# Optimization experiments

Measured on AMD Instinct MI355X. Metric: run time of the kernel, lower is better.

## Reference

```python
import jax, jax.numpy as jnp
import numpy as np

B, L, D_MODEL = 2, 2048, 1024
D_INNER, D_STATE, D_CONV, DT_RANK = 2048, 16, 4, 64


def setup_inputs() -> dict:
    key = jax.random.key(0)
    ks = jax.random.split(key, 20)
    g = lambda k, shape, s: (jax.random.normal(k, shape, jnp.float32) * s)
    A_init = jnp.log(jnp.broadcast_to(
        jnp.arange(1, D_STATE + 1, dtype=jnp.float32), (D_INNER, D_STATE)))
    inp = {
        "hidden": g(ks[0], (B, L, D_MODEL), 1.0),
        # tied across directions (bidirectional_weight_tie=True)
        "W_in": g(ks[1], (2 * D_INNER, D_MODEL), 0.02),
        "W_out": g(ks[2], (D_MODEL, D_INNER), 0.02),
        # forward-direction Mamba params
        "conv_w_f": g(ks[3], (D_INNER, D_CONV), 0.2),
        "conv_b_f": jnp.zeros((D_INNER,), jnp.float32),
        "W_x_f": g(ks[4], (DT_RANK + 2 * D_STATE, D_INNER), 0.02),
        "W_dt_f": g(ks[5], (D_INNER, DT_RANK), 0.05),
        "b_dt_f": jax.random.uniform(ks[6], (D_INNER,), jnp.float32, -5.0, -4.0),
        "A_log_f": A_init,
        "D_f": jnp.ones((D_INNER,), jnp.float32),
        # reverse-direction Mamba params
        "conv_w_r": g(ks[7], (D_INNER, D_CONV), 0.2),
        "conv_b_r": jnp.zeros((D_INNER,), jnp.float32),
        "W_x_r": g(ks[8], (DT_RANK + 2 * D_STATE, D_INNER), 0.02),
        "W_dt_r": g(ks[9], (D_INNER, DT_RANK), 0.05),
        "b_dt_r": jax.random.uniform(ks[10], (D_INNER,), jnp.float32, -5.0, -4.0),
        "A_log_r": A_init,
        "D_r": jnp.ones((D_INNER,), jnp.float32),
    }
    return inp


def _mamba_block(h, W_in, W_out, conv_w, conv_b, W_x, W_dt, b_dt, A_log, Dp):
    # h: (B, L, d_model)
    xz = jnp.einsum('bld,ed->ble', h, W_in)          # (B,L,2*d_inner)
    x, z = jnp.split(xz, 2, axis=-1)
    # depthwise causal conv over L
    ker = jnp.swapaxes(conv_w, 0, 1)[:, None, :]      # (d_conv,1,d_inner)
    xc = jax.lax.conv_general_dilated(
        x, ker, window_strides=(1,), padding=[(D_CONV - 1, 0)],
        dimension_numbers=('NWC', 'WIO', 'NWC'),
        feature_group_count=D_INNER) + conv_b
    u = jax.nn.silu(xc)                               # (B,L,d_inner)
    xdbl = jnp.einsum('bld,ed->ble', u, W_x)          # (B,L,r+2n)
    dt, Bm, Cm = jnp.split(xdbl, [DT_RANK, DT_RANK + D_STATE], axis=-1)
    delta = jax.nn.softplus(jnp.einsum('blr,dr->bld', dt, W_dt) + b_dt)
    A = -jnp.exp(A_log)                               # (d_inner,d_state)

    def step(hs, xs):
        d_t, B_t, C_t, u_t = xs                       # (B,di),(B,n),(B,n),(B,di)
        dA = jnp.exp(d_t[:, :, None] * A)             # (B,di,n)
        hs = hs * dA + (d_t * u_t)[:, :, None] * B_t[:, None, :]
        y_t = jnp.einsum('bdn,bn->bd', hs, C_t)
        return hs, y_t

    xs = (jnp.swapaxes(delta, 0, 1), jnp.swapaxes(Bm, 0, 1),
          jnp.swapaxes(Cm, 0, 1), jnp.swapaxes(u, 0, 1))
    h0 = jnp.zeros((h.shape[0], D_INNER, D_STATE), h.dtype)
    _, ys = jax.lax.scan(step, h0, xs)                # ys: (L,B,d_inner)
    y = jnp.swapaxes(ys, 0, 1) + u * Dp
    y = y * jax.nn.silu(z)
    return jnp.einsum('bld,od->blo', y, W_out)        # (B,L,d_model)


def reference(hidden, W_in, W_out,
              conv_w_f, conv_b_f, W_x_f, W_dt_f, b_dt_f, A_log_f, D_f,
              conv_w_r, conv_b_r, W_x_r, W_dt_r, b_dt_r, A_log_r, D_r):
    out_f = _mamba_block(hidden, W_in, W_out, conv_w_f, conv_b_f,
                         W_x_f, W_dt_f, b_dt_f, A_log_f, D_f)
    out_r = _mamba_block(jnp.flip(hidden, axis=1), W_in, W_out, conv_w_r,
                         conv_b_r, W_x_r, W_dt_r, b_dt_r, A_log_r, D_r)
    return out_f + jnp.flip(out_r, axis=1)            # bidirectional 'add'
```

## Files before the change

kernel.cpp:

```cpp
#include <hip/hip_runtime.h>
#include <hip/hip_bf16.h>
#include <math.h>

typedef unsigned short u16;
typedef __attribute__((ext_vector_type(8))) short short8_t;
typedef __attribute__((ext_vector_type(4))) float f32x4;

#define B_   2
#define L_   2048
#define DM_  1024
#define DI_  2048
#define DS_  16
#define DR_  64
#define G_   96
#define BL_  (B_*L_)
#define BLDI_ ((size_t)BL_*DI_)
#define BLG_  ((size_t)BL_*G_)
#define NSEG_ 64
#define SEG_  32
#define PSTR_ ((size_t)BL_*G_)

__device__ __forceinline__ float sigmoidf_(float x){ return 1.f/(1.f+__expf(-x)); }
__device__ __forceinline__ float siluf_(float x){ return x*sigmoidf_(x); }
__device__ __forceinline__ float softplusf_(float x){
    return fmaxf(x,0.f) + __logf(1.f + __expf(-fabsf(x)));
}
__device__ __forceinline__ float bf2f(u16 u){
    union{unsigned int i; float f;} c; c.i = ((unsigned int)u)<<16; return c.f;
}
__device__ __forceinline__ u16 f2bf(float v){
    __hip_bfloat16 h = __float2bfloat16(v); return *(u16*)&h;
}
__device__ __forceinline__ void gll16(const void* g, void* l){
    __builtin_amdgcn_global_load_lds(
        (const __attribute__((address_space(1))) unsigned int*)g,
        (__attribute__((address_space(3))) unsigned int*)l, 16, 0, 0);
}
#define SCHUNK(lane) ((((lane) & 3) - (((lane) >> 3) & 3)) & 3)

__global__ __launch_bounds__(256) void f2ball_kernel(
    const float* __restrict__ p0, u16* __restrict__ q0,
    const float* __restrict__ p1, u16* __restrict__ q1,
    const float* __restrict__ p2, u16* __restrict__ q2,
    const float* __restrict__ p3, u16* __restrict__ q3,
    const float* __restrict__ p4, u16* __restrict__ q4,
    const float* __restrict__ p5, u16* __restrict__ q5,
    const float* __restrict__ p6, u16* __restrict__ q6)
{
    unsigned i = blockIdx.x*256 + threadIdx.x;
    const float* src; u16* dst; unsigned j;
    if      (i < 1048576u)            { src=p0; dst=q0; j=i; }
    else if (i < 2097152u)            { src=p1; dst=q1; j=i-1048576u; }
    else if (i < 2146304u)            { src=p2; dst=q2; j=i-2097152u; }
    else if (i < 2195456u)            { src=p3; dst=q3; j=i-2146304u; }
    else if (i < 2228224u)            { src=p4; dst=q4; j=i-2195456u; }
    else if (i < 2260992u)            { src=p5; dst=q5; j=i-2228224u; }
    else                              { src=p6; dst=q6; j=i-2260992u; }
    float4 v = *(const float4*)(src + (size_t)j*4);
    u16 t[4] = { f2bf(v.x), f2bf(v.y), f2bf(v.z), f2bf(v.w) };
    *(ushort4*)(dst + (size_t)j*4) = *(const ushort4*)t;
}

#define ABUF_ (128*64)
#define TBUF_ (ABUF_ + 256*64)

template<int C0, int C1>
__device__ __forceinline__ void stage256(
    const u16* __restrict__ A, int lda,
    const u16* __restrict__ B, int ldb,
    int m0, int n0, int k0, u16* buf,
    int wave, int lr, int cg)
{
    #pragma unroll
    for (int c = C0; c < C1; ++c) {
        if (c < 2) {
            const int r = wave*16 + c*8;
            gll16(A + (size_t)(m0 + r + lr)*lda + k0 + cg, buf + r*64);
        } else {
            const int r = wave*32 + (c-2)*8;
            gll16(B + (size_t)(n0 + r + lr)*ldb + k0 + cg, buf + ABUF_ + r*64);
        }
    }
}

__global__ __launch_bounds__(512, 2) void gemm256(
    const u16* __restrict__ A, int lda,
    const u16* __restrict__ B, int ldb,
    u16* __restrict__ C2, float* __restrict__ Cf, size_t cfZStr,
    int ldc, int K)
{
    __shared__ __align__(16) u16 lds3[3][TBUF_];

    const int tid  = threadIdx.x;
    const int wave = tid >> 6, lane = tid & 63;
    const int quad = lane >> 4, l16 = lane & 15;
    const int wm = wave >> 2, wn = wave & 3;
    const int m0 = blockIdx.y * 128, n0 = blockIdx.x * 256;
    const int nk = K >> 6;
    const int ks = blockIdx.z;
    A += (size_t)ks * K;
    B += (size_t)ks * K;

    const int lr  = lane >> 3;
    const int cg  = ((lane & 7) ^ lr) << 3;
    const int csw = l16 & 7;

    f32x4 acc[4][4];
    #pragma unroll
    for (int i = 0; i < 4; ++i)
        #pragma unroll
        for (int j = 0; j < 4; ++j) acc[i][j] = (f32x4){0.f,0.f,0.f,0.f};

    stage256<0,6>(A, lda, B, ldb, m0, n0, 0, lds3[0], wave, lr, cg);
    if (nk > 1)
        stage256<0,6>(A, lda, B, ldb, m0, n0, 64, lds3[1], wave, lr, cg);

    for (int t = 0; t < nk; ++t) {
        const u16* rb = lds3[t % 3];
        u16* sb = lds3[(t + 2) % 3];
        const int k2 = (t + 2) << 6;

        __builtin_amdgcn_sched_barrier(0);
        if (t + 1 < nk) asm volatile("s_waitcnt vmcnt(6)" ::: "memory");
        else            asm volatile("s_waitcnt vmcnt(0)" ::: "memory");
        __builtin_amdgcn_sched_barrier(0);
        __builtin_amdgcn_s_barrier();

        short8_t af[4][2], bf[4][2];
        #pragma unroll
        for (int i = 0; i < 4; ++i)
            #pragma unroll
            for (int kk = 0; kk < 2; ++kk)
                af[i][kk] = *(const short8_t*)
                    &rb[(wm*64 + i*16 + l16)*64 + (((kk*4+quad)^csw)<<3)];
        #pragma unroll
        for (int j = 0; j < 2; ++j)
            #pragma unroll
            for (int kk = 0; kk < 2; ++kk)
                bf[j][kk] = *(const short8_t*)
                    &rb[ABUF_ + (wn*64 + j*16 + l16)*64 + (((kk*4+quad)^csw)<<3)];
        if (t + 2 < nk)
            stage256<0,3>(A, lda, B, ldb, m0, n0, k2, sb, wave, lr, cg);
        asm volatile("s_waitcnt lgkmcnt(0)" ::: "memory");
        __builtin_amdgcn_sched_barrier(0);
        __builtin_amdgcn_s_setprio(1);
        #pragma unroll
        for (int i = 0; i < 4; ++i)
            #pragma unroll
            for (int j = 0; j < 2; ++j)
                #pragma unroll
                for (int kk = 0; kk < 2; ++kk)
                    acc[i][j] = __builtin_amdgcn_mfma_f32_16x16x32_bf16(
                                    bf[j][kk], af[i][kk], acc[i][j], 0, 0, 0);
        __builtin_amdgcn_s_setprio(0);
        __builtin_amdgcn_s_barrier();

        #pragma unroll
        for (int j = 2; j < 4; ++j)
            #pragma unroll
            for (int kk = 0; kk < 2; ++kk)
                bf[j][kk] = *(const short8_t*)
                    &rb[ABUF_ + (wn*64 + j*16 + l16)*64 + (((kk*4+quad)^csw)<<3)];
        if (t + 2 < nk)
            stage256<3,6>(A, lda, B, ldb, m0, n0, k2, sb, wave, lr, cg);
        asm volatile("s_waitcnt lgkmcnt(0)" ::: "memory");
        __builtin_amdgcn_sched_barrier(0);
        __builtin_amdgcn_s_setprio(1);
        #pragma unroll
        for (int i = 0; i < 4; ++i)
            #pragma unroll
            for (int j = 2; j < 4; ++j)
                #pragma unroll
                for (int kk = 0; kk < 2; ++kk)
                    acc[i][j] = __builtin_amdgcn_mfma_f32_16x16x32_bf16(
                                    bf[j][kk], af[i][kk], acc[i][j], 0, 0, 0);
        __builtin_amdgcn_s_setprio(0);
    }

    if (Cf) {
        float* dst = Cf + (size_t)ks*cfZStr;
        #pragma unroll
        for (int i = 0; i < 4; ++i) {
            const int row = m0 + wm*64 + i*16 + l16;
            #pragma unroll
            for (int j = 0; j < 4; ++j) {
                const int col = n0 + wn*64 + j*16 + quad*4;
                *(float4*)&dst[(size_t)row*ldc + col] =
                    make_float4(acc[i][j][0], acc[i][j][1],
                                acc[i][j][2], acc[i][j][3]);
            }
        }
    } else {
        #pragma unroll
        for (int i = 0; i < 4; ++i) {
            const int row = m0 + wm*64 + i*16 + l16;
            #pragma unroll
            for (int j = 0; j < 4; ++j) {
                const int col = n0 + wn*64 + j*16 + quad*4;
                u16 t4[4] = { f2bf(acc[i][j][0]), f2bf(acc[i][j][1]),
                              f2bf(acc[i][j][2]), f2bf(acc[i][j][3]) };
                *(ushort4*)&C2[(size_t)row*ldc + col] = *(const ushort4*)t4;
            }
        }
    }
}

__global__ __launch_bounds__(256) void wred_kernel(
    const float* __restrict__ P, float* __restrict__ out)
{
    unsigned i = blockIdx.x*256 + threadIdx.x;
    size_t o = (size_t)i*4;
    float4 a = *(const float4*)&P[o];
    float4 b = *(const float4*)&P[o + (size_t)BL_*DM_];
    a.x += b.x; a.y += b.y; a.z += b.z; a.w += b.w;
    *(float4*)&out[o] = a;
}

__global__ __launch_bounds__(256) void gemm_mfma(
    const u16* __restrict__ A, int lda, size_t aStr,
    const u16* __restrict__ B, int ldb, size_t bStr,
    float* __restrict__ C, int ldc, size_t cStr,
    u16* __restrict__ C2,
    int M, int N, int K,
    const float* __restrict__ bias0, const float* __restrict__ bias1, int epi)
{
    __shared__ u16 Al[128*32];
    __shared__ u16 Bl[128*32];

    const int dir = blockIdx.z;
    A += (size_t)dir*aStr; B += (size_t)dir*bStr;
    if (C)  C  += (size_t)dir*cStr;
    if (C2) C2 += (size_t)dir*cStr;
    const float* bias = dir ? bias1 : bias0;

    const int tid  = threadIdx.x;
    const int wave = tid >> 6, lane = tid & 63;
    const int wm = (wave >> 1) * 64, wn = (wave & 1) * 64;
    const int m0 = blockIdx.y * 128, n0 = blockIdx.x * 128;
    const int quad = lane >> 4, l16 = lane & 15;

    const int srow = lane >> 2;
    const int scol = SCHUNK(lane) * 8;
    const int rc0  = ((quad + (l16 >> 1)) & 3) * 8;

    f32x4 acc[4][4];
    #pragma unroll
    for (int i = 0; i < 4; ++i)
        #pragma unroll
        for (int j = 0; j < 4; ++j) acc[i][j] = (f32x4){0.f,0.f,0.f,0.f};

    for (int k0 = 0; k0 < K; k0 += 32) {
        __syncthreads();
        #pragma unroll
        for (int j = 0; j < 2; ++j) {
            const int g   = wave*2 + j;
            const int row = g*16 + srow;
            gll16(A + (size_t)(m0 + row)*lda + k0 + scol, &Al[g*16*32]);
            gll16(B + (size_t)(n0 + row)*ldb + k0 + scol, &Bl[g*16*32]);
        }
        __syncthreads();

        short8_t af[4], bf[4];
        #pragma unroll
        for (int i = 0; i < 4; ++i) {
            af[i] = *(const short8_t*)&Al[(wm + i*16 + l16)*32 + rc0];
            bf[i] = *(const short8_t*)&Bl[(wn + i*16 + l16)*32 + rc0];
        }
        #pragma unroll
        for (int i = 0; i < 4; ++i)
            #pragma unroll
            for (int j = 0; j < 4; ++j)
                acc[i][j] = __builtin_amdgcn_mfma_f32_16x16x32_bf16(
                                bf[j], af[i], acc[i][j], 0, 0, 0);
    }

    #pragma unroll
    for (int i = 0; i < 4; ++i) {
        const int row = m0 + wm + i*16 + l16;
        #pragma unroll
        for (int j = 0; j < 4; ++j) {
            const int col = n0 + wn + j*16 + quad*4;
            if (col < N) {
                float4 o = make_float4(acc[i][j][0], acc[i][j][1],
                                       acc[i][j][2], acc[i][j][3]);
                if (epi) {
                    float4 bb = *(const float4*)&bias[col];
                    o.x = softplusf_(o.x + bb.x);
                    o.y = softplusf_(o.y + bb.y);
                    o.z = softplusf_(o.z + bb.z);
                    o.w = softplusf_(o.w + bb.w);
                }
                if (C) *(float4*)&C[(size_t)row*ldc + col] = o;
                if (C2) {
                    u16 t[4] = { f2bf(o.x), f2bf(o.y), f2bf(o.z), f2bf(o.w) };
                    *(ushort4*)&C2[(size_t)row*ldc + col] = *(const ushort4*)t;
                }
            }
        }
    }
}

__global__ __launch_bounds__(256) void gemm_mfma64(
    const u16* __restrict__ A, int lda, size_t aStr,
    const u16* __restrict__ B, int ldb, size_t bStr,
    float* __restrict__ C, int ldc, size_t cZStr,
    int M, int N, int Ksub, int KS)
{
    __shared__ u16 Al[64*32];
    __shared__ u16 Bl[128*32];

    const int z = blockIdx.z;
    const int dir = z / KS, ks = z - dir*KS;
    A += (size_t)dir*aStr + (size_t)ks*Ksub;
    B += (size_t)dir*bStr + (size_t)ks*Ksub;
    C += (size_t)z*cZStr;

    const int tid  = threadIdx.x;
    const int wave = tid >> 6, lane = tid & 63;
    const int m0 = blockIdx.y * 64, n0 = blockIdx.x * 128;
    const int quad = lane >> 4, l16 = lane & 15;
    const int wn = wave * 32;

    const int srow = lane >> 2;
    const int scol = SCHUNK(lane) * 8;
    const int rc0  = ((quad + (l16 >> 1)) & 3) * 8;

    f32x4 acc[4][2];
    #pragma unroll
    for (int i = 0; i < 4; ++i)
        #pragma unroll
        for (int j = 0; j < 2; ++j) acc[i][j] = (f32x4){0.f,0.f,0.f,0.f};

    for (int k0 = 0; k0 < Ksub; k0 += 32) {
        __syncthreads();
        gll16(A + (size_t)(m0 + wave*16 + srow)*lda + k0 + scol, &Al[wave*16*32]);
        #pragma unroll
        for (int j = 0; j < 2; ++j) {
            const int g = wave*2 + j;
            gll16(B + (size_t)(n0 + g*16 + srow)*ldb + k0 + scol, &Bl[g*16*32]);
        }
        __syncthreads();

        short8_t af[4], bf[2];
        #pragma unroll
        for (int i = 0; i < 4; ++i)
            af[i] = *(const short8_t*)&Al[(i*16 + l16)*32 + rc0];
        #pragma unroll
        for (int j = 0; j < 2; ++j)
            bf[j] = *(const short8_t*)&Bl[(wn + j*16 + l16)*32 + rc0];
        #pragma unroll
        for (int i = 0; i < 4; ++i)
            #pragma unroll
            for (int j = 0; j < 2; ++j)
                acc[i][j] = __builtin_amdgcn_mfma_f32_16x16x32_bf16(
                                bf[j], af[i], acc[i][j], 0, 0, 0);
    }

    #pragma unroll
    for (int i = 0; i < 4; ++i) {
        const int row = m0 + i*16 + l16;
        #pragma unroll
        for (int j = 0; j < 2; ++j) {
            const int col = n0 + wn + j*16 + quad*4;
            if (col < N) {
                float4 o = make_float4(acc[i][j][0], acc[i][j][1],
                                       acc[i][j][2], acc[i][j][3]);
                *(float4*)&C[(size_t)row*ldc + col] = o;
            }
        }
    }
}

__global__ __launch_bounds__(256) void xred_kernel(
    const float* __restrict__ P, float* __restrict__ XD, u16* __restrict__ XDb)
{
    unsigned i = blockIdx.x*256 + threadIdx.x;
    unsigned c4  = i % 24;
    unsigned row = (i / 24) & 4095;
    unsigned dir = i / (24*4096);
    size_t o = (size_t)row*G_ + c4*4;
    size_t pb = (size_t)dir*4*PSTR_ + o;

    float4 s = *(const float4*)&P[pb];
    #pragma unroll
    for (int ks = 1; ks < 4; ++ks) {
        float4 v = *(const float4*)&P[pb + (size_t)ks*PSTR_];
        s.x += v.x; s.y += v.y; s.z += v.z; s.w += v.w;
    }
    *(float4*)&XD[(size_t)dir*BLG_ + o] = s;
    u16 t[4] = { f2bf(s.x), f2bf(s.y), f2bf(s.z), f2bf(s.w) };
    *(ushort4*)&XDb[(size_t)dir*BLG_ + o] = *(const ushort4*)t;
}

#define LPT_ 8
__global__ __launch_bounds__(256) void conv_silu_kernel(
    const u16* __restrict__ xz,
    const float* __restrict__ wf, const float* __restrict__ bf_,
    const float* __restrict__ wr, const float* __restrict__ br_,
    u16* __restrict__ ub)
{
    unsigned i = blockIdx.x*256 + threadIdx.x;
    int d0  = (i & 511) << 2;
    int lg  = (i >> 9) & 255;
    int b   = (i >> 17) & 1;
    int dir = (int)(i >> 18);

    const float* wv = dir ? wr : wf;
    const float* bv = dir ? br_ : bf_;
    float4 bias = *(const float4*)(bv + d0);
    float4 w0 = *(const float4*)(wv + (d0+0)*4);
    float4 w1 = *(const float4*)(wv + (d0+1)*4);
    float4 w2 = *(const float4*)(wv + (d0+2)*4);
    float4 w3 = *(const float4*)(wv + (d0+3)*4);

    const int l0 = lg * LPT_;
    const size_t xb = (size_t)b*L_*4096 + d0;

    float h0[4], h1[4], h2[4];
    #pragma unroll
    for (int c = 0; c < 4; ++c) { h0[c]=0.f; h1[c]=0.f; h2[c]=0.f; }
    if (lg > 0) {
        #pragma unroll
        for (int k = 0; k < 3; ++k) {
            int j = l0 - 3 + k;
            int row = dir ? (L_-1-j) : j;
            uint2 xr = *(const uint2*)(&xz[xb + (size_t)row*4096]);
            const u16* xp = (const u16*)&xr;
            float* h = (k==0) ? h0 : ((k==1) ? h1 : h2);
            h[0]=bf2f(xp[0]); h[1]=bf2f(xp[1]); h[2]=bf2f(xp[2]); h[3]=bf2f(xp[3]);
        }
    }

    size_t off = (((size_t)dir*B_ + b)*L_ + l0)*DI_ + d0;
    #pragma unroll
    for (int t = 0; t < LPT_; ++t) {
        int j = l0 + t;
        int row = dir ? (L_-1-j) : j;
        uint2 xr = *(const uint2*)(&xz[xb + (size_t)row*4096]);
        const u16* xp = (const u16*)&xr;
        float c0 = bf2f(xp[0]), c1 = bf2f(xp[1]);
        float c2 = bf2f(xp[2]), c3 = bf2f(xp[3]);
        float a0 = bias.x + h0[0]*w0.x + h1[0]*w0.y + h2[0]*w0.z + c0*w0.w;
        float a1 = bias.y + h0[1]*w1.x + h1[1]*w1.y + h2[1]*w1.z + c1*w1.w;
        float a2 = bias.z + h0[2]*w2.x + h1[2]*w2.y + h2[2]*w2.z + c2*w2.w;
        float a3 = bias.w + h0[3]*w3.x + h1[3]*w3.y + h2[3]*w3.z + c3*w3.w;
        u16 t4[4] = { f2bf(siluf_(a0)), f2bf(siluf_(a1)),
                      f2bf(siluf_(a2)), f2bf(siluf_(a3)) };
        *(ushort4*)(ub + off) = *(const ushort4*)t4;
        off += DI_;
        #pragma unroll
        for (int c = 0; c < 4; ++c) { h0[c]=h1[c]; h1[c]=h2[c]; }
        h2[0]=c0; h2[1]=c1; h2[2]=c2; h2[3]=c3;
    }
}

__device__ __forceinline__ void scan_ld16(
    const u16* __restrict__ dp, const u16* __restrict__ up, int c,
    u16 (&dr)[16], u16 (&ur)[16])
{
    #pragma unroll
    for (int j = 0; j < 16; ++j) {
        dr[j] = dp[(size_t)((c<<4)+j)*DI_];
        ur[j] = up[(size_t)((c<<4)+j)*DI_];
    }
}

__device__ __forceinline__ void scanA_chunk16(
    const u16 (&dr)[16], const u16 (&ur)[16], int rbase,
    float (&h)[16], float& sumd, const float (*sB)[DS_])
{
    #pragma unroll
    for (int li = 0; li < 16; ++li) {
        const int row = rbase + li;
        float dlt = bf2f(dr[li]);
        float du  = dlt * bf2f(ur[li]);
        sumd += dlt;
        float e1 = __expf(-dlt);
        float e2 = e1*e1, e3 = e2*e1, e4 = e2*e2;
        float g5 = e1*e4, g6 = e2*e4, g7 = e3*e4, g8 = e4*e4;
        float g9 = e1*g8, g10 = e2*g8, g11 = e3*g8, g12 = e4*g8;
        float g13 = g5*g8, g14 = g6*g8, g15 = g7*g8, g16 = g8*g8;
        const float4* bp = (const float4*)&sB[row][0];
        float4 B0 = bp[0], B1 = bp[1], B2 = bp[2], B3 = bp[3];
        h[0]  = h[0] *e1  + du*B0.x;  h[1]  = h[1] *e2  + du*B0.y;
        h[2]  = h[2] *e3  + du*B0.z;  h[3]  = h[3] *e4  + du*B0.w;
        h[4]  = h[4] *g5  + du*B1.x;  h[5]  = h[5] *g6  + du*B1.y;
        h[6]  = h[6] *g7  + du*B1.z;  h[7]  = h[7] *g8  + du*B1.w;
        h[8]  = h[8] *g9  + du*B2.x;  h[9]  = h[9] *g10 + du*B2.y;
        h[10] = h[10]*g11 + du*B2.z;  h[11] = h[11]*g12 + du*B2.w;
        h[12] = h[12]*g13 + du*B3.x;  h[13] = h[13]*g14 + du*B3.y;
        h[14] = h[14]*g15 + du*B3.z;  h[15] = h[15]*g16 + du*B3.w;
    }
}

__device__ __forceinline__ void scanB_chunk16(
    const u16 (&dr)[16], const u16 (&ur)[16], int rbase,
    float (&h)[16], const float (*sB)[DS_], const float (*sC)[DS_],
    u16* __restrict__ yp)
{
    #pragma unroll
    for (int li = 0; li < 16; ++li) {
        const int row = rbase + li;
        float dlt = bf2f(dr[li]);
        float du  = dlt * bf2f(ur[li]);
        float e1 = __expf(-dlt);
        float e2 = e1*e1, e3 = e2*e1, e4 = e2*e2;
        float g5 = e1*e4, g6 = e2*e4, g7 = e3*e4, g8 = e4*e4;
        float g9 = e1*g8, g10 = e2*g8, g11 = e3*g8, g12 = e4*g8;
        float g13 = g5*g8, g14 = g6*g8, g15 = g7*g8, g16 = g8*g8;
        const float4* bp = (const float4*)&sB[row][0];
        const float4* cp = (const float4*)&sC[row][0];
        float4 B0 = bp[0], B1 = bp[1], B2 = bp[2], B3 = bp[3];
        float4 C0 = cp[0], C1 = cp[1], C2v = cp[2], C3 = cp[3];
        h[0]  = h[0] *e1  + du*B0.x;  h[1]  = h[1] *e2  + du*B0.y;
        h[2]  = h[2] *e3  + du*B0.z;  h[3]  = h[3] *e4  + du*B0.w;
        h[4]  = h[4] *g5  + du*B1.x;  h[5]  = h[5] *g6  + du*B1.y;
        h[6]  = h[6] *g7  + du*B1.z;  h[7]  = h[7] *g8  + du*B1.w;
        h[8]  = h[8] *g9  + du*B2.x;  h[9]  = h[9] *g10 + du*B2.y;
        h[10] = h[10]*g11 + du*B2.z;  h[11] = h[11]*g12 + du*B2.w;
        h[12] = h[12]*g13 + du*B3.x;  h[13] = h[13]*g14 + du*B3.y;
        h[14] = h[14]*g15 + du*B3.z;  h[15] = h[15]*g16 + du*B3.w;
        float y0 = h[0]*C0.x  + h[1]*C0.y  + h[2]*C0.z  + h[3]*C0.w;
        float y1 = h[4]*C1.x  + h[5]*C1.y  + h[6]*C1.z  + h[7]*C1.w;
        float y2 = h[8]*C2v.x + h[9]*C2v.y + h[10]*C2v.z+ h[11]*C2v.w;
        float y3 = h[12]*C3.x + h[13]*C3.y + h[14]*C3.z + h[15]*C3.w;
        yp[(size_t)row*DI_] = f2bf((y0+y1)+(y2+y3));
    }
}

__global__ __launch_bounds__(256) void scan_passA(
    const u16* __restrict__ ub,
    const u16* __restrict__ db,
    const float* __restrict__ xdbl,
    float* __restrict__ Hend, float* __restrict__ Sd)
{
    __shared__ float sB[SEG_][DS_];

    const int bx  = blockIdx.x;
    const int seg = bx & 63, dg = (bx >> 6) & 7, pair = bx >> 9;
    const int tid = threadIdx.x;
    const int d   = (dg << 8) + tid;
    const int lseg = seg * SEG_;
    const size_t base  = (size_t)pair * L_ * DI_;
    const size_t xbase = (size_t)pair * L_ * G_;

    const u16* dp = db + base + (size_t)lseg*DI_ + d;
    const u16* up = ub + base + (size_t)lseg*DI_ + d;

    u16 dr0[16], ur0[16], dr1[16], ur1[16];
    scan_ld16(dp, up, 0, dr0, ur0);
    scan_ld16(dp, up, 1, dr1, ur1);

    #pragma unroll
    for (int k = 0; k < 2; ++k) {
        int idx = (k << 8) + tid;
        sB[idx >> 4][idx & 15] =
            xdbl[xbase + (size_t)(lseg + (idx >> 4))*G_ + 64 + (idx & 15)];
    }

    float h[16];
    #pragma unroll
    for (int n = 0; n < 16; ++n) h[n] = 0.f;
    float sumd = 0.f;
    __syncthreads();

    scanA_chunk16(dr0, ur0,  0, h, sumd, sB);
    scanA_chunk16(dr1, ur1, 16, h, sumd, sB);

    const size_t ho = ((size_t)(seg*4 + pair)*2048 + d)*16;
    #pragma unroll
    for (int r = 0; r < 4; ++r)
        *(float4*)&Hend[ho + r*4] = make_float4(h[r*4],h[r*4+1],h[r*4+2],h[r*4+3]);
    Sd[(size_t)(seg*4 + pair)*2048 + d] = sumd;
}

__global__ __launch_bounds__(256) void scan_fixup(
    const float* __restrict__ Hend, const float* __restrict__ Sd,
    float* __restrict__ Hin,
    const float* __restrict__ A_log_f, const float* __restrict__ A_log_r)
{
    int idx = blockIdx.x*256 + threadIdx.x;
    int n = idx & 15, d = (idx >> 4) & 2047, pair = idx >> 15;
    int dir = pair >> 1;
    float a = -__expf((dir ? A_log_r : A_log_f)[d*16 + n]);
    float hin = 0.f;
    #pragma unroll
    for (int s = 0; s < NSEG_; ++s) {
        size_t o = ((size_t)(s*4 + pair)*2048 + d)*16 + n;
        Hin[o] = hin;
        float P = __expf(a * Sd[(size_t)(s*4 + pair)*2048 + d]);
        hin = Hend[o] + P*hin;
    }
}

__global__ __launch_bounds__(256) void scan_passB(
    const u16* __restrict__ ub,
    const u16* __restrict__ db,
    const float* __restrict__ xdbl,
    const float* __restrict__ Hin,
    u16* __restrict__ yb)
{
    __shared__ float sB[SEG_][DS_];
    __shared__ float sC[SEG_][DS_];

    const int bx  = blockIdx.x;
    const int seg = bx & 63, dg = (bx >> 6) & 7, pair = bx >> 9;
    const int tid = threadIdx.x;
    const int d   = (dg << 8) + tid;
    const int lseg = seg * SEG_;
    const size_t base  = (size_t)pair * L_ * DI_;
    const size_t xbase = (size_t)pair * L_ * G_;

    const u16* dp = db + base + (size_t)lseg*DI_ + d;
    const u16* up = ub + base + (size_t)lseg*DI_ + d;
    u16*       yp = yb + base + (size_t)lseg*DI_ + d;

    u16 dr0[16], ur0[16], dr1[16], ur1[16];
    scan_ld16(dp, up, 0, dr0, ur0);
    scan_ld16(dp, up, 1, dr1, ur1);

    #pragma unroll
    for (int k = 0; k < 2; ++k) {
        int idx = (k << 8) + tid;
        int row = idx >> 4, col = idx & 15;
        const float* src = &xdbl[xbase + (size_t)(lseg + row)*G_ + 64 + col];
        sB[row][col] = src[0];
        sC[row][col] = src[16];
    }

    float h[16];
    const size_t ho = ((size_t)(seg*4 + pair)*2048 + d)*16;
    #pragma unroll
    for (int r = 0; r < 4; ++r) {
        float4 v = *(const float4*)&Hin[ho + r*4];
        h[r*4]=v.x; h[r*4+1]=v.y; h[r*4+2]=v.z; h[r*4+3]=v.w;
    }
    __syncthreads();

    scanB_chunk16(dr0, ur0,  0, h, sB, sC, yp);
    scanB_chunk16(dr1, ur1, 16, h, sB, sC, yp);
}

__global__ __launch_bounds__(256) void combine_kernel(
    const u16* __restrict__ xz,
    const u16* __restrict__ ub,
    const u16* __restrict__ yb,
    const float* __restrict__ Df, const float* __restrict__ Dr,
    u16* __restrict__ cb)
{
    unsigned i = blockIdx.x*256 + threadIdx.x;
    int d0 = (i & 511) << 2;
    int l  = (i >> 9) & (L_-1);
    int b  = (int)(i >> 20);
    size_t row  = (size_t)b*L_ + l;
    size_t rowp = (size_t)b*L_ + (L_-1 - l);

    uint2 zr  = *(const uint2*)(&xz[row*4096 + 2048 + d0]);
    uint2 yfr = *(const uint2*)(&yb[row*DI_ + d0]);
    uint2 yrr = *(const uint2*)(&yb[BLDI_ + rowp*DI_ + d0]);
    uint2 ufr = *(const uint2*)(&ub[row*DI_ + d0]);
    uint2 urr = *(const uint2*)(&ub[BLDI_ + rowp*DI_ + d0]);
    float4 Dfv = *(const float4*)(Df + d0);
    float4 Drv = *(const float4*)(Dr + d0);
    const u16* zp = (const u16*)&zr;
    const u16* yf = (const u16*)&yfr;
    const u16* yr = (const u16*)&yrr;
    const u16* uf = (const u16*)&ufr;
    const u16* ur = (const u16*)&urr;
    const float* Dfp = (const float*)&Dfv;
    const float* Drp = (const float*)&Drv;

    u16 t4[4];
    #pragma unroll
    for (int k = 0; k < 4; ++k) {
        float v = (bf2f(yf[k]) + bf2f(uf[k])*Dfp[k])
                + (bf2f(yr[k]) + bf2f(ur[k])*Drp[k]);
        t4[k] = f2bf(v * siluf_(bf2f(zp[k])));
    }
    *(ushort4*)(cb + row*DI_ + d0) = *(const ushort4*)t4;
}

extern "C" void kernel_launch(void* const* d_in, const int* in_sizes, int n_in,
                              void* d_out, int out_size, void* d_ws, size_t ws_size,
                              hipStream_t stream)
{
    const float* hidden = (const float*)d_in[0];
    const float* W_in   = (const float*)d_in[1];
    const float* W_out  = (const float*)d_in[2];
    const float* cwf    = (const float*)d_in[3];
    const float* cbf    = (const float*)d_in[4];
    const float* Wxf    = (const float*)d_in[5];
    const float* Wdtf   = (const float*)d_in[6];
    const float* bdtf   = (const float*)d_in[7];
    const float* Alf    = (const float*)d_in[8];
    const float* Dfp    = (const float*)d_in[9];
    const float* cwr    = (const float*)d_in[10];
    const float* cbr    = (const float*)d_in[11];
    const float* Wxr    = (const float*)d_in[12];
    const float* Wdtr   = (const float*)d_in[13];
    const float* bdtr   = (const float*)d_in[14];
    const float* Alr    = (const float*)d_in[15];
    const float* Drp    = (const float*)d_in[16];
    float* out = (float*)d_out;

    char* w = (char*)d_ws;
    u16*   XZb  = (u16*)  (w);
    u16*   Ub   = (u16*)  (w + (32u<<20));
    u16*   Db   = (u16*)  (w + (64u<<20));
    float* Pw   = (float*)(w + (64u<<20));
    u16*   Yb   = (u16*)  (w + (96u<<20));
    float* Sd   = (float*)(w + (96u<<20));
    float* Hin  = (float*)(w + (128u<<20));
    float* P    = (float*)(w + (128u<<20));
    u16*   Cb   = (u16*)  (w + (128u<<20));
    float* Hend = (float*)(w + (160u<<20));
    u16*   hb   = (u16*)  (w + (160u<<20));
    u16*   Winb = (u16*)  (w + (168u<<20));
    float* XD   = (float*)(w + (192u<<20));
    u16*   XDb  = (u16*)  (w + (195u<<20));
    u16*   Wxb  = (u16*)  (w + (196u<<20) + (512u<<10));
    u16*   Wdtb = (u16*)  (w + (197u<<20) + (256u<<10));
    u16*   Wob  = (u16*)  (w + (197u<<20) + (768u<<10));

    dim3 blk(256);

    f2ball_kernel<<<10880,blk,0,stream>>>(hidden,hb, W_in,Winb,
                                          Wxf,Wxb, Wxr,Wxb+196608,
                                          Wdtf,Wdtb, Wdtr,Wdtb+131072,
                                          W_out,Wob);
    gemm256<<<dim3(16,32,1),dim3(512),0,stream>>>(hb,DM_, Winb,DM_,
                                                  XZb, nullptr,0, 2*DI_, DM_);
    conv_silu_kernel<<<2048,blk,0,stream>>>(XZb,cwf,cbf,cwr,cbr,Ub);
    gemm_mfma64<<<dim3(1,64,8),blk,0,stream>>>(Ub,DI_,BLDI_, Wxb,DI_,196608,
                                               P,G_,PSTR_, BL_,G_,DI_/4,4);
    xred_kernel<<<768,blk,0,stream>>>(P, XD, XDb);
    gemm_mfma<<<dim3(16,32,2),blk,0,stream>>>(XDb,G_,BLG_, Wdtb,DR_,131072,
                                              nullptr,DI_,BLDI_, Db,
                                              BL_,DI_,DR_, bdtf,bdtr,1);
    scan_passA<<<2048,blk,0,stream>>>(Ub, Db, XD, Hend, Sd);
    scan_fixup<<<512,blk,0,stream>>>(Hend, Sd, Hin, Alf, Alr);
    scan_passB<<<2048,blk,0,stream>>>(Ub, Db, XD, Hin, Yb);
    combine_kernel<<<8192,blk,0,stream>>>(XZb, Ub, Yb, Dfp, Drp, Cb);
    gemm256<<<dim3(4,32,2),dim3(512),0,stream>>>(Cb,DI_, Wob,DI_,
                                                 nullptr, Pw,(size_t)BL_*DM_,
                                                 DM_, DI_/2);
    wred_kernel<<<4096,blk,0,stream>>>(Pw, out);
}
```

Baseline: 351.3 us.

## Replace input projection GEMM with 256x256-tile double-buffered pipelined MFMA kernel

Adds a new bf16 GEMM kernel for the input projection that uses 256x256 output tiles per 512-thread block. It double-buffers 64-wide K slices in LDS with swizzled direct global-to-LDS loads interleaved between MFMA phases, using explicit waitcnt, barriers and setprio. The goal is to hide global-load latency behind MFMA work and raise data reuse per tile compared with the prior gemm256 launch. In exchange it uses much larger per-block LDS and register footprints and launches fewer blocks (256 instead of 512), which may lower occupancy or leave some CUs idle.

```diff
diff --git a/kernel.cpp b/kernel.cpp
--- a/kernel.cpp
+++ b/kernel.cpp
@@ -59,6 +59,148 @@
     float4 v = *(const float4*)(src + (size_t)j*4);
     u16 t[4] = { f2bf(v.x), f2bf(v.y), f2bf(v.z), f2bf(v.w) };
     *(ushort4*)(dst + (size_t)j*4) = *(const ushort4*)t;
+}
+
+#define XSL_ 8192
+#define XA_  (2*XSL_)
+
+__device__ __forceinline__ void st8p(
+    const u16* __restrict__ M, int ldm, int gr0, int kcol,
+    u16* __restrict__ dst, int wave, int srow, int schunk)
+{
+    #pragma unroll
+    for (int n = 0; n < 2; ++n) {
+        const int rbw = wave*32 + n*16;
+        gll16(M + (size_t)(gr0 + rbw + srow)*ldm + kcol + schunk*8,
+              dst + rbw*32);
+    }
+}
+
+__global__ __launch_bounds__(512, 2) void gemm8p(
+    const u16* __restrict__ A, int lda,
+    const u16* __restrict__ B, int ldb,
+    u16* __restrict__ C2, int ldc, int K)
+{
+    __shared__ __align__(16) u16 lds2[2][2*XA_];
+
+    const int tid  = threadIdx.x;
+    const int wave = tid >> 6, lane = tid & 63;
+    const int quad = lane >> 4, l16 = lane & 15;
+    const int wm = wave >> 2, wn = wave & 3;
+    const int m0 = blockIdx.y * 256, n0 = blockIdx.x * 256;
+    const int nt = K >> 6;
+
+    const int srow   = lane >> 2;
+    const int schunk = (lane & 3) ^ (srow & 3);
+    const int rchunk = (quad ^ (l16 & 3)) * 8;
+
+    f32x4 acc[8][4];
+    #pragma unroll
+    for (int i = 0; i < 8; ++i)
+        #pragma unroll
+        for (int j = 0; j < 4; ++j) acc[i][j] = (f32x4){0.f,0.f,0.f,0.f};
+
+    st8p(A, lda, m0, 0,  (u16*)&lds2[0][0],          wave, srow, schunk);
+    st8p(B, ldb, n0, 0,  (u16*)&lds2[0][XA_],        wave, srow, schunk);
+    st8p(A, lda, m0, 32, (u16*)&lds2[0][XSL_],       wave, srow, schunk);
+    st8p(B, ldb, n0, 32, (u16*)&lds2[0][XA_ + XSL_], wave, srow, schunk);
+
+    for (int t = 0; t < nt; ++t) {
+        const u16* rb = lds2[t & 1];
+        u16* sb = (u16*)lds2[(t + 1) & 1];
+        const int kc = (t + 1) << 6;
+        const bool more = (t + 1) < nt;
+
+        const int arow = (wm*128 + l16)*32 + rchunk;
+        const int brow = XA_ + (wn*64 + l16)*32 + rchunk;
+
+        short8_t af[8], bf0, bf1;
+
+        __builtin_amdgcn_sched_barrier(0);
+        asm volatile("s_waitcnt vmcnt(4)" ::: "memory");
+        __builtin_amdgcn_sched_barrier(0);
+        __builtin_amdgcn_s_barrier();
+
+        #pragma unroll
+        for (int i = 0; i < 8; ++i)
+            af[i] = *(const short8_t*)&rb[arow + i*512];
+        bf0 = *(const short8_t*)&rb[brow + 0*512];
+        bf1 = *(const short8_t*)&rb[brow + 1*512];
+        if (more) st8p(A, lda, m0, kc, sb, wave, srow, schunk);
+        __builtin_amdgcn_s_barrier();
+        asm volatile("s_waitcnt lgkmcnt(0)" ::: "memory");
+        __builtin_amdgcn_sched_barrier(0);
+        __builtin_amdgcn_s_setprio(1);
+        #pragma unroll
+        for (int i = 0; i < 8; ++i) {
+            acc[i][0] = __builtin_amdgcn_mfma_f32_16x16x32_bf16(bf0, af[i], acc[i][0], 0,0,0);
+            acc[i][1] = __builtin_amdgcn_mfma_f32_16x16x32_bf16(bf1, af[i], acc[i][1], 0,0,0);
+        }
+        __builtin_amdgcn_s_setprio(0);
+        __builtin_amdgcn_s_barrier();
+
+        bf0 = *(const short8_t*)&rb[brow + 2*512];
+        bf1 = *(const short8_t*)&rb[brow + 3*512];
+        if (more) st8p(B, ldb, n0, kc, sb + XA_, wave, srow, schunk);
+        asm volatile("s_waitcnt lgkmcnt(0)" ::: "memory");
+        __builtin_amdgcn_sched_barrier(0);
+        __builtin_amdgcn_s_setprio(1);
+        #pragma unroll
+        for (int i = 0; i < 8; ++i) {
+            acc[i][2] = __builtin_amdgcn_mfma_f32_16x16x32_bf16(bf0, af[i], acc[i][2], 0,0,0);
+            acc[i][3] = __builtin_amdgcn_mfma_f32_16x16x32_bf16(bf1, af[i], acc[i][3], 0,0,0);
+        }
+        __builtin_amdgcn_s_setprio(0);
+
+        __builtin_amdgcn_sched_barrier(0);
+        if (more) asm volatile("s_waitcnt vmcnt(4)" ::: "memory");
+        else      asm volatile("s_waitcnt vmcnt(0)" ::: "memory");
+        __builtin_amdgcn_sched_barrier(0);
+        __builtin_amdgcn_s_barrier();
+
+        #pragma unroll
+        for (int i = 0; i < 8; ++i)
+            af[i] = *(const short8_t*)&rb[XSL_ + arow + i*512];
+        bf0 = *(const short8_t*)&rb[XSL_ + brow + 0*512];
+        bf1 = *(const short8_t*)&rb[XSL_ + brow + 1*512];
+        if (more) st8p(A, lda, m0, kc + 32, sb + XSL_, wave, srow, schunk);
+        __builtin_amdgcn_s_barrier();
+        asm volatile("s_waitcnt lgkmcnt(0)" ::: "memory");
+        __builtin_amdgcn_sched_barrier(0);
+        __builtin_amdgcn_s_setprio(1);
+        #pragma unroll
+        for (int i = 0; i < 8; ++i) {
+            acc[i][0] = __builtin_amdgcn_mfma_f32_16x16x32_bf16(bf0, af[i], acc[i][0], 0,0,0);
+            acc[i][1] = __builtin_amdgcn_mfma_f32_16x16x32_bf16(bf1, af[i], acc[i][1], 0,0,0);
+        }
+        __builtin_amdgcn_s_setprio(0);
+        __builtin_amdgcn_s_barrier();
+
+        bf0 = *(const short8_t*)&rb[XSL_ + brow + 2*512];
+        bf1 = *(const short8_t*)&rb[XSL_ + brow + 3*512];
+        if (more) st8p(B, ldb, n0, kc + 32, sb + XA_ + XSL_, wave, srow, schunk);
+        asm volatile("s_waitcnt lgkmcnt(0)" ::: "memory");
+        __builtin_amdgcn_sched_barrier(0);
+        __builtin_amdgcn_s_setprio(1);
+        #pragma unroll
+        for (int i = 0; i < 8; ++i) {
+            acc[i][2] = __builtin_amdgcn_mfma_f32_16x16x32_bf16(bf0, af[i], acc[i][2], 0,0,0);
+            acc[i][3] = __builtin_amdgcn_mfma_f32_16x16x32_bf16(bf1, af[i], acc[i][3], 0,0,0);
+        }
+        __builtin_amdgcn_s_setprio(0);
+    }
+
+    #pragma unroll
+    for (int i = 0; i < 8; ++i) {
+        const int row = m0 + wm*128 + i*16 + l16;
+        #pragma unroll
+        for (int j = 0; j < 4; ++j) {
+            const int col = n0 + wn*64 + j*16 + quad*4;
+            u16 t4[4] = { f2bf(acc[i][j][0]), f2bf(acc[i][j][1]),
+                          f2bf(acc[i][j][2]), f2bf(acc[i][j][3]) };
+            *(ushort4*)&C2[(size_t)row*ldc + col] = *(const ushort4*)t4;
+        }
+    }
 }
 
 #define ABUF_ (128*64)
@@ -728,8 +870,8 @@
                                           Wxf,Wxb, Wxr,Wxb+196608,
                                           Wdtf,Wdtb, Wdtr,Wdtb+131072,
                                           W_out,Wob);
-    gemm256<<<dim3(16,32,1),dim3(512),0,stream>>>(hb,DM_, Winb,DM_,
-                                                  XZb, nullptr,0, 2*DI_, DM_);
+    gemm8p<<<dim3(16,16),dim3(512),0,stream>>>(hb,DM_, Winb,DM_,
+                                               XZb, 2*DI_, DM_);
     conv_silu_kernel<<<2048,blk,0,stream>>>(XZb,cwf,cbf,cwr,cbr,Ub);
     gemm_mfma64<<<dim3(1,64,8),blk,0,stream>>>(Ub,DI_,BLDI_, Wxb,DI_,196608,
                                                P,G_,PSTR_, BL_,G_,DI_/4,4);
```

After: 354.2 us. Within noise of the previous version (+0.8%).
